# Kernel tuning notes

Measured on AMD Instinct MI355X. Metric: run time of the kernel, lower is better.

## Reference

```python
import jax, jax.numpy as jnp
import numpy as np

L, S, M, N, E, H = 1024, 1024, 256, 8, 512, 8


def embed_rotary(x, cos, sin):
    # x: [B, T, E]; interleaved rotate-half as in RotaryPositionEncoding.embed_rotary
    x2 = jnp.stack([-x[..., 1::2], x[..., 0::2]], axis=-1).reshape(x.shape)
    return x * cos + x2 * sin


def setup_inputs() -> dict:
    key = jax.random.key(0)
    ks = jax.random.split(key, 12)
    return {
        "query": jax.random.normal(ks[0], (L, N, E), jnp.float32),
        "key": jax.random.normal(ks[1], (S, N, E), jnp.float32),
        "value": jax.random.normal(ks[2], (S, N, E), jnp.float32),
        "in_proj_weight": jax.random.normal(ks[3], (3 * E, E), jnp.float32) / np.sqrt(E).astype(np.float32),
        "in_proj_bias": jnp.zeros((3 * E,), jnp.float32),
        "out_proj_weight": jax.random.normal(ks[4], (E, E), jnp.float32) / np.sqrt(E).astype(np.float32),
        "out_proj_bias": jnp.zeros((E,), jnp.float32),
        "rot_q": jax.random.normal(ks[5], (N, L, E, 2), jnp.float32),
        "rot_k": jax.random.normal(ks[6], (N, S, E, 2), jnp.float32),
        "k_mem": jax.random.normal(ks[7], (M, N, E), jnp.float32),
        "v_mem": jax.random.normal(ks[8], (M, N, E), jnp.float32),
        "gate_attn": jax.random.normal(ks[9], (H,), jnp.float32),
        "mem_mask": jax.random.randint(ks[10], (N, M), 0, 2).astype(bool),
        "num_heads": H,
    }


def reference(query, key, value, in_proj_weight, in_proj_bias, out_proj_weight,
              out_proj_bias, rot_q, rot_k, k_mem, v_mem, gate_attn, mem_mask, num_heads):
    L_, N_, E_ = query.shape
    S_ = key.shape[0]
    H_ = num_heads
    hd = E_ // H_
    scale = float(hd) ** -0.5
    # separate q/k/v projections (qkv not identical path)
    q = query @ in_proj_weight[:E_].T + in_proj_bias[:E_]
    k = key @ in_proj_weight[E_:2 * E_].T + in_proj_bias[E_:2 * E_]
    v = value @ in_proj_weight[2 * E_:].T + in_proj_bias[2 * E_:]
    q = q * scale
    # inline rotary PE (applied in batch-first layout, then back)
    q = embed_rotary(q.transpose(1, 0, 2), rot_q[..., 0], rot_q[..., 1]).transpose(1, 0, 2)
    k = embed_rotary(k.transpose(1, 0, 2), rot_k[..., 0], rot_k[..., 1]).transpose(1, 0, 2)
    qh = q.reshape(L_, N_, H_, hd).transpose(1, 2, 0, 3)  # [N,H,L,hd]
    kh = k.reshape(S_, N_, H_, hd).transpose(1, 2, 0, 3)  # [N,H,S,hd]
    vh = v.reshape(S_, N_, H_, hd).transpose(1, 2, 0, 3)
    scores = jnp.einsum('nhld,nhsd->nhls', qh, kh)
    # slot-competition: softmax over queries (slots), then renormalize over keys
    w = jax.nn.softmax(scores, axis=2) + 1e-8
    w = w / w.sum(axis=-1, keepdims=True)
    attn = jnp.einsum('nhls,nhsd->nhld', w, vh)
    # memorizing-transformer style memory K/V branch with sigmoid head gating
    Mm = k_mem.shape[0]
    km = k_mem.reshape(Mm, N_, H_, hd).transpose(1, 2, 0, 3)  # [N,H,M,hd]
    vm = v_mem.reshape(Mm, N_, H_, hd).transpose(1, 2, 0, 3)
    sm = jnp.einsum('nhld,nhmd->nhlm', qh, km)
    sm = jnp.where(mem_mask[:, None, None, :], -1e9, sm)  # additive -inf mask
    wm = jax.nn.softmax(sm, axis=-1)
    om = jnp.einsum('nhlm,nhmd->nhld', wm, vm)
    gate = jax.nn.sigmoid(gate_attn)[None, :, None, None]  # [1,H,1,1]
    attn = gate * om + (1.0 - gate) * attn
    out = attn.transpose(2, 0, 1, 3).reshape(L_, N_, E_)  # back to [L,N,E]
    return out @ out_proj_weight.T + out_proj_bias
```

## Files before the change

kernel.cpp:

```cpp
#include <hip/hip_runtime.h>
#include <hip/hip_bf16.h>

typedef __hip_bfloat16 bf16;
typedef __bf16 bf16x8 __attribute__((ext_vector_type(8)));
typedef float f32x4 __attribute__((ext_vector_type(4)));

#define LQ 1024
#define SK 1024
#define MMEM 256
#define NB 8
#define EE 512
#define NH 8
#define HD 64
#define NBH 64

__device__ inline __bf16 tobf(float f) {
  __hip_bfloat16 h = __float2bfloat16(f);
  return *reinterpret_cast<__bf16*>(&h);
}
__device__ inline float bf2f(__bf16 x) {
  unsigned short u; __builtin_memcpy(&u, &x, 2);
  unsigned int v = (unsigned int)u << 16;
  float f; __builtin_memcpy(&f, &v, 4);
  return f;
}
__device__ inline f32x4 MFMA(bf16x8 a, bf16x8 b, f32x4 c) {
  return __builtin_amdgcn_mfma_f32_16x16x32_bf16(a, b, c, 0, 0, 0);
}

__device__ inline void gload_lds16(const bf16* g, void* l) {
  __builtin_amdgcn_global_load_lds(
      (const __attribute__((address_space(1))) void*)g,
      (__attribute__((address_space(3))) void*)l, 16, 0, 0);
}

__device__ inline bf16x8 load8(const float* p) {
  float4 a = *(const float4*)p;
  float4 b = *(const float4*)(p + 4);
  bf16x8 r;
  r[0] = tobf(a.x); r[1] = tobf(a.y); r[2] = tobf(a.z); r[3] = tobf(a.w);
  r[4] = tobf(b.x); r[5] = tobf(b.y); r[6] = tobf(b.z); r[7] = tobf(b.w);
  return r;
}

#define CVT_T0 524288
#define CVT_T3 98304
#define CVT_T4 32768
__global__ __launch_bounds__(256) void convert5(
    const float* __restrict__ q, const float* __restrict__ k,
    const float* __restrict__ v, const float* __restrict__ w,
    const float* __restrict__ o, bf16* __restrict__ qc, bf16* __restrict__ kc,
    bf16* __restrict__ vc, bf16* __restrict__ wc, bf16* __restrict__ oc)
{
  long long t = (long long)blockIdx.x * 256 + threadIdx.x;
  const float* src; bf16* dst; long long idx;
  if (t < CVT_T0)               { src = q; dst = qc; idx = t; }
  else if (t < 2 * CVT_T0)      { src = k; dst = kc; idx = t - CVT_T0; }
  else if (t < 3 * CVT_T0)      { src = v; dst = vc; idx = t - 2 * CVT_T0; }
  else if (t < 3 * CVT_T0 + CVT_T3) { src = w; dst = wc; idx = t - 3 * CVT_T0; }
  else                          { src = o; dst = oc; idx = t - 3 * CVT_T0 - CVT_T3; }
  *(bf16x8*)(dst + idx * 8) = load8(src + idx * 8);
}

__global__ __launch_bounds__(256) void gemm_proj3(
    const bf16* __restrict__ qc, const bf16* __restrict__ kc,
    const bf16* __restrict__ vc, const bf16* __restrict__ ipwb,
    const float* __restrict__ ipb, bf16* __restrict__ pq,
    bf16* __restrict__ pk, bf16* __restrict__ v_raw)
{
  __shared__ __align__(16) char smem[33792];
  __bf16* As = (__bf16*)smem;
  __bf16* Bs = (__bf16*)(smem + 16384);
  const int z = blockIdx.z;
  const bf16* A = (z == 0) ? qc : (z == 1) ? kc : vc;
  const bf16* W = ipwb + (long long)z * EE * EE;
  const float* bias = ipb + z * EE;
  const float alpha = (z == 0) ? 0.125f : 1.f;
  const int bid2 = blockIdx.y * gridDim.x + blockIdx.x;
  const int xcd = bid2 & 7, sub = bid2 >> 3;
  const int by = (xcd << 3) + (sub >> 2);
  const int bx = sub & 3;
  const int tm0 = by << 7, tn0 = bx << 7;
  const int t = threadIdx.x;
  const int wave = t >> 6, lane = t & 63;
  const int wrow0 = (wave & 1) << 6, wcol0 = (wave >> 1) << 6;
  const int m16 = lane & 15, quad = lane >> 4;

  const f32x4 zero = {0.f, 0.f, 0.f, 0.f};
  f32x4 acc[4][4];
#pragma unroll
  for (int mi = 0; mi < 4; ++mi)
#pragma unroll
    for (int ni = 0; ni < 4; ++ni) acc[mi][ni] = zero;

  const bf16* Ab = A + (long long)tm0 * EE;
  const bf16* Bb = W + (long long)tn0 * EE;
  const int ob_u = wave << 10;

  for (int k0 = 0; k0 < EE; k0 += 64) {
#pragma unroll
    for (int c = 0; c < 4; ++c) {
      int ob = (c << 12) + ob_u;
      int obl = ob + (lane << 4);
      int row = obl >> 7;
      int ce = (obl & 127) >> 1;
      gload_lds16(Ab + (long long)row * EE + k0 + ce, smem + ob);
      gload_lds16(Bb + (long long)row * EE + k0 + ce, smem + 16384 + ob);
    }
    __syncthreads();
#pragma unroll
    for (int kh = 0; kh < 2; ++kh) {
      bf16x8 av[4], bv[4];
#pragma unroll
      for (int i = 0; i < 4; ++i) {
        av[i] = *(bf16x8*)(As + ((wrow0 + (i << 4) + m16) << 6) + (kh << 5) + (quad << 3));
        bv[i] = *(bf16x8*)(Bs + ((wcol0 + (i << 4) + m16) << 6) + (kh << 5) + (quad << 3));
      }
#pragma unroll
      for (int mi = 0; mi < 4; ++mi)
#pragma unroll
        for (int ni = 0; ni < 4; ++ni)
          acc[mi][ni] = MFMA(av[mi], bv[ni], acc[mi][ni]);
    }
    __syncthreads();
  }

  __bf16 (*Cs)[132] = (__bf16(*)[132])smem;
#pragma unroll
  for (int mi = 0; mi < 4; ++mi)
#pragma unroll
    for (int ni = 0; ni < 4; ++ni) {
      int col = wcol0 + (ni << 4) + m16;
      float bv = bias[tn0 + col];
#pragma unroll
      for (int r = 0; r < 4; ++r)
        Cs[wrow0 + (mi << 4) + (quad << 2) + r][col] =
            tobf((acc[mi][ni][r] + bv) * alpha);
    }
  __syncthreads();
  bf16* O = (z == 0) ? pq : (z == 1) ? pk : v_raw;
  const int crow = t >> 1, ch0 = (t & 1) << 6;
  long long gb = (long long)(tm0 + crow) * EE + tn0 + ch0;
#pragma unroll
  for (int j = 0; j < 64; j += 8)
    *(uint4*)(O + gb + j) = *(uint4*)&Cs[crow][ch0 + j];
}

__global__ __launch_bounds__(256) void rotary_kernel(
    const bf16* __restrict__ pq, const bf16* __restrict__ pk,
    const float* __restrict__ rot_q, const float* __restrict__ rot_k,
    bf16* __restrict__ Qh, bf16* __restrict__ Kh)
{
  const bf16* src = blockIdx.y ? pk : pq;
  const float* rot = blockIdx.y ? rot_k : rot_q;
  bf16* dst = blockIdx.y ? Kh : Qh;
  const int t = threadIdx.x;
  const int row = (blockIdx.x << 2) + (t >> 6);
  const int e0 = (t & 63) << 3;
  const int l = row >> 3, n = row & 7;
  bf16x8 x = *(const bf16x8*)(src + (long long)row * EE + e0);
  const float* rp = rot + ((((long long)n * LQ + l) * EE + e0) << 1);
  __bf16 vals[8];
#pragma unroll
  for (int j = 0; j < 8; j += 2) {
    float4 cs4 = *(const float4*)(rp + (j << 1));
    float x0 = bf2f(x[j]);
    float x1 = bf2f(x[j + 1]);
    vals[j]     = tobf(x0 * cs4.x - x1 * cs4.y);
    vals[j + 1] = tobf(x1 * cs4.z + x0 * cs4.w);
  }
  const int h = e0 >> 6, d0 = e0 & 63;
  *(uint4*)(dst + (((long long)(n * NH + h) * LQ + l) * HD + d0)) = *(uint4*)vals;
}

__global__ __launch_bounds__(256) void colsum_kernel(
    const bf16* __restrict__ Qh, const bf16* __restrict__ Kh,
    float* __restrict__ csum)
{
  __shared__ __align__(16) char QdB[16384];
  __shared__ float cpart[128][2];
  const int bid = blockIdx.y * gridDim.x + blockIdx.x;
  const int xcd = bid & 7, sub = bid >> 3;
  const int b = (xcd << 3) + (sub >> 3);
  const int st0 = (sub & 7) << 7;
  const int t = threadIdx.x;
  const int wave = t >> 6, lane = t & 63;
  const int wm = (wave & 1) << 5, wn = (wave >> 1) << 5;
  const int m16 = lane & 15, quad = lane >> 4;
  const int swz = (m16 & 7) << 4;

  bf16x8 bk[2][2][2];
#pragma unroll
  for (int g = 0; g < 2; ++g)
#pragma unroll
    for (int ni = 0; ni < 2; ++ni)
#pragma unroll
      for (int kh = 0; kh < 2; ++kh)
        bk[g][ni][kh] = *(const bf16x8*)(
            Kh + ((long long)b * SK + st0 + (g << 6) + wn + (ni << 4) + m16) * HD
               + (kh << 5) + (quad << 3));

  int ldsoff[2]; const bf16* qsrc[2];
#pragma unroll
  for (int c = 0; c < 2; ++c) {
    int tb = (wave << 11) + (c << 10) + (lane << 4);
    int row = tb >> 7, cb = tb & 127;
    int srcb = cb ^ ((row & 7) << 4);
    ldsoff[c] = (wave << 11) + (c << 10);
    qsrc[c] = Qh + ((long long)b * LQ + row) * HD + (srcb >> 1);
  }
#pragma unroll
  for (int c = 0; c < 2; ++c) gload_lds16(qsrc[c], QdB + ldsoff[c]);
  __syncthreads();

  const f32x4 zero = {0.f, 0.f, 0.f, 0.f};
  float colp[2][2] = {{0.f, 0.f}, {0.f, 0.f}};
  int cur = 0;
  for (int lt = 0; lt < 16; ++lt) {
    if (lt < 15) {
#pragma unroll
      for (int c = 0; c < 2; ++c)
        gload_lds16(qsrc[c] + (long long)(lt + 1) * 64 * HD,
                    QdB + ((cur ^ 1) << 13) + ldsoff[c]);
    }
    bf16x8 a0k[2], a1k[2];
#pragma unroll
    for (int kh = 0; kh < 2; ++kh) {
      int byt = ((kh << 6) + (quad << 4)) ^ swz;
      a0k[kh] = *(bf16x8*)(QdB + (cur << 13) + (wm + m16) * 128 + byt);
      a1k[kh] = *(bf16x8*)(QdB + (cur << 13) + (wm + 16 + m16) * 128 + byt);
    }
    f32x4 s[2][2][2];
#pragma unroll
    for (int g = 0; g < 2; ++g)
#pragma unroll
      for (int mi = 0; mi < 2; ++mi)
#pragma unroll
        for (int ni = 0; ni < 2; ++ni) s[g][mi][ni] = zero;
    __builtin_amdgcn_s_setprio(1);
#pragma unroll
    for (int g = 0; g < 2; ++g)
#pragma unroll
      for (int kh = 0; kh < 2; ++kh) {
        s[g][0][0] = MFMA(a0k[kh], bk[g][0][kh], s[g][0][0]);
        s[g][0][1] = MFMA(a0k[kh], bk[g][1][kh], s[g][0][1]);
        s[g][1][0] = MFMA(a1k[kh], bk[g][0][kh], s[g][1][0]);
        s[g][1][1] = MFMA(a1k[kh], bk[g][1][kh], s[g][1][1]);
      }
    __builtin_amdgcn_s_setprio(0);
#pragma unroll
    for (int g = 0; g < 2; ++g)
#pragma unroll
      for (int mi = 0; mi < 2; ++mi)
#pragma unroll
        for (int ni = 0; ni < 2; ++ni)
#pragma unroll
          for (int r = 0; r < 4; ++r)
            colp[g][ni] += __expf(s[g][mi][ni][r]);
    __syncthreads();
    cur ^= 1;
  }
#pragma unroll
  for (int g = 0; g < 2; ++g)
#pragma unroll
    for (int ni = 0; ni < 2; ++ni) {
      float v = colp[g][ni];
      v += __shfl_down(v, 32, 64);
      v += __shfl_down(v, 16, 64);
      if (quad == 0) cpart[(g << 6) + wn + (ni << 4) + m16][wm >> 5] = v;
    }
  __syncthreads();
  if (t < 128) csum[b * SK + st0 + t] = cpart[t][0] + cpart[t][1];
}

__global__ __launch_bounds__(256) void attn_fused(
    const bf16* __restrict__ Qh, const bf16* __restrict__ Kh,
    const bf16* __restrict__ Vt, const bf16* __restrict__ km,
    const bf16* __restrict__ vmt, const float* __restrict__ csum,
    const float* __restrict__ Vsum, const int* __restrict__ mask,
    const float* __restrict__ gate, bf16* __restrict__ comb)
{
  __shared__ __align__(16) char KdB[16384];
  __shared__ __align__(16) char VdB[16384];
  __shared__ __align__(16) char PsB[8192];
  __shared__ __align__(16) float rcs[SK];
  __shared__ __align__(16) float mskf[MMEM];
  __shared__ float rpa[64][2];
  __shared__ float rpm[64][2];
  const int bid = blockIdx.y * gridDim.x + blockIdx.x;
  const int xcd = bid & 7, sub = bid >> 3;
  const int b = (xcd << 3) + (sub >> 4);
  const int tm0 = (sub & 15) << 6;
  const int n = b >> 3, h = b & 7;
  const int t = threadIdx.x;
  const int lrow = t >> 2, lcol = (t & 3) << 4;
  const int wave = t >> 6, lane = t & 63;
  const int wm = (wave & 1) << 5, wn = (wave >> 1) << 5;
  const int m16 = lane & 15, quad = lane >> 4;
  const int swz = (m16 & 7) << 4;

#pragma unroll
  for (int i = 0; i < 4; ++i)
    rcs[t + i * 256] = 1.f / csum[b * SK + t + i * 256];
  mskf[t] = mask[n * MMEM + t] ? 0.f : 1.f;

  bf16x8 aq[2][2];
#pragma unroll
  for (int li = 0; li < 2; ++li)
#pragma unroll
    for (int kh = 0; kh < 2; ++kh)
      aq[li][kh] = *(const bf16x8*)(
          Qh + ((long long)b * LQ + tm0 + wm + (li << 4) + m16) * HD
             + (kh << 5) + (quad << 3));

  int ldsoff[2]; int srow[2], scol[2];
#pragma unroll
  for (int c = 0; c < 2; ++c) {
    int tb = (wave << 11) + (c << 10) + (lane << 4);
    int row = tb >> 7, cb = tb & 127;
    int srcb = cb ^ ((row & 7) << 4);
    ldsoff[c] = (wave << 11) + (c << 10);
    srow[c] = row; scol[c] = srcb >> 1;
  }
  const bf16* kmain = Kh + (long long)b * SK * HD;
  const bf16* vmain = Vt + (long long)b * HD * SK;
  const bf16* kmem = km + (long long)b * MMEM * HD;
  const bf16* vmem = vmt + (long long)b * HD * MMEM;

#pragma unroll
  for (int c = 0; c < 2; ++c) {
    gload_lds16(kmem + (long long)srow[c] * HD + scol[c], KdB + ldsoff[c]);
    gload_lds16(vmem + (long long)srow[c] * MMEM + scol[c], VdB + ldsoff[c]);
  }
  __syncthreads();

  const f32x4 zero = {0.f, 0.f, 0.f, 0.f};
  f32x4 m00 = zero, m01 = zero, m10 = zero, m11 = zero;
  f32x4 o00 = zero, o01 = zero, o10 = zero, o11 = zero;
  float rsm[2] = {0.f, 0.f};
  float rsa[2] = {0.f, 0.f};
  int cur = 0;

  for (int mt = 0; mt < 4; ++mt) {
    if (mt < 3) {
#pragma unroll
      for (int c = 0; c < 2; ++c) {
        gload_lds16(kmem + ((long long)((mt + 1) << 6) + srow[c]) * HD + scol[c],
                    KdB + ((cur ^ 1) << 13) + ldsoff[c]);
        gload_lds16(vmem + (long long)srow[c] * MMEM + ((mt + 1) << 6) + scol[c],
                    VdB + ((cur ^ 1) << 13) + ldsoff[c]);
      }
    } else {
#pragma unroll
      for (int c = 0; c < 2; ++c) {
        gload_lds16(kmain + (long long)srow[c] * HD + scol[c],
                    KdB + ((cur ^ 1) << 13) + ldsoff[c]);
        gload_lds16(vmain + (long long)srow[c] * SK + scol[c],
                    VdB + ((cur ^ 1) << 13) + ldsoff[c]);
      }
    }
    f32x4 s00 = zero, s01 = zero, s10 = zero, s11 = zero;
    __builtin_amdgcn_s_setprio(1);
#pragma unroll
    for (int kh = 0; kh < 2; ++kh) {
      int byt = ((kh << 6) + (quad << 4)) ^ swz;
      bf16x8 ak0 = *(bf16x8*)(KdB + (cur << 13) + (wn + m16) * 128 + byt);
      bf16x8 ak1 = *(bf16x8*)(KdB + (cur << 13) + (wn + 16 + m16) * 128 + byt);
      s00 = MFMA(ak0, aq[0][kh], s00);
      s01 = MFMA(ak0, aq[1][kh], s01);
      s10 = MFMA(ak1, aq[0][kh], s10);
      s11 = MFMA(ak1, aq[1][kh], s11);
    }
    __builtin_amdgcn_s_setprio(0);
    {
      char* pA = PsB + (wm + m16) * 128;
      char* pB = PsB + (wm + 16 + m16) * 128;
#pragma unroll
      for (int si = 0; si < 2; ++si) {
        int sloc = wn + (si << 4) + (quad << 2);
        f32x4 mf4 = *(const f32x4*)&mskf[(mt << 6) + sloc];
        f32x4 sA = si ? s10 : s00;
        f32x4 sB = si ? s11 : s01;
        __bf16 vA[4], vB[4];
#pragma unroll
        for (int r = 0; r < 4; ++r) {
          float pa = __expf(sA[r]) * mf4[r];
          rsm[0] += pa; vA[r] = tobf(pa);
          float pb = __expf(sB[r]) * mf4[r];
          rsm[1] += pb; vB[r] = tobf(pb);
        }
        int sbyte = (sloc << 1) ^ swz;
        *(uint2*)(pA + sbyte) = *(uint2*)vA;
        *(uint2*)(pB + sbyte) = *(uint2*)vB;
      }
    }
    __syncthreads();
    __builtin_amdgcn_s_setprio(1);
#pragma unroll
    for (int kh = 0; kh < 2; ++kh) {
      int sb = (kh << 6) + (quad << 4);
      int byt = sb ^ swz;
      bf16x8 ap0 = *(bf16x8*)(PsB + (wm + m16) * 128 + byt);
      bf16x8 ap1 = *(bf16x8*)(PsB + (wm + 16 + m16) * 128 + byt);
      bf16x8 bv0 = *(bf16x8*)(VdB + (cur << 13) + (wn + m16) * 128 + byt);
      bf16x8 bv1 = *(bf16x8*)(VdB + (cur << 13) + (wn + 16 + m16) * 128 + byt);
      m00 = MFMA(ap0, bv0, m00);
      m01 = MFMA(ap0, bv1, m01);
      m10 = MFMA(ap1, bv0, m10);
      m11 = MFMA(ap1, bv1, m11);
    }
    __builtin_amdgcn_s_setprio(0);
    __syncthreads();
    cur ^= 1;
  }

  for (int st = 0; st < 16; ++st) {
    if (st < 15) {
#pragma unroll
      for (int c = 0; c < 2; ++c) {
        gload_lds16(kmain + ((long long)((st + 1) << 6) + srow[c]) * HD + scol[c],
                    KdB + ((cur ^ 1) << 13) + ldsoff[c]);
        gload_lds16(vmain + (long long)srow[c] * SK + ((st + 1) << 6) + scol[c],
                    VdB + ((cur ^ 1) << 13) + ldsoff[c]);
      }
    }
    f32x4 s00 = zero, s01 = zero, s10 = zero, s11 = zero;
    __builtin_amdgcn_s_setprio(1);
#pragma unroll
    for (int kh = 0; kh < 2; ++kh) {
      int byt = ((kh << 6) + (quad << 4)) ^ swz;
      bf16x8 ak0 = *(bf16x8*)(KdB + (cur << 13) + (wn + m16) * 128 + byt);
      bf16x8 ak1 = *(bf16x8*)(KdB + (cur << 13) + (wn + 16 + m16) * 128 + byt);
      s00 = MFMA(ak0, aq[0][kh], s00);
      s01 = MFMA(ak0, aq[1][kh], s01);
      s10 = MFMA(ak1, aq[0][kh], s10);
      s11 = MFMA(ak1, aq[1][kh], s11);
    }
    __builtin_amdgcn_s_setprio(0);
    {
      char* pA = PsB + (wm + m16) * 128;
      char* pB = PsB + (wm + 16 + m16) * 128;
#pragma unroll
      for (int si = 0; si < 2; ++si) {
        int sloc = wn + (si << 4) + (quad << 2);
        f32x4 rc4 = *(const f32x4*)&rcs[(st << 6) + sloc];
        f32x4 sA = si ? s10 : s00;
        f32x4 sB = si ? s11 : s01;
        __bf16 vA[4], vB[4];
#pragma unroll
        for (int r = 0; r < 4; ++r) {
          float pa = __expf(sA[r]) * rc4[r];
          rsa[0] += pa; vA[r] = tobf(pa);
          float pb = __expf(sB[r]) * rc4[r];
          rsa[1] += pb; vB[r] = tobf(pb);
        }
        int sbyte = (sloc << 1) ^ swz;
        *(uint2*)(pA + sbyte) = *(uint2*)vA;
        *(uint2*)(pB + sbyte) = *(uint2*)vB;
      }
    }
    __syncthreads();
    __builtin_amdgcn_s_setprio(1);
#pragma unroll
    for (int kh = 0; kh < 2; ++kh) {
      int sb = (kh << 6) + (quad << 4);
      int byt = sb ^ swz;
      bf16x8 ap0 = *(bf16x8*)(PsB + (wm + m16) * 128 + byt);
      bf16x8 ap1 = *(bf16x8*)(PsB + (wm + 16 + m16) * 128 + byt);
      bf16x8 bv0 = *(bf16x8*)(VdB + (cur << 13) + (wn + m16) * 128 + byt);
      bf16x8 bv1 = *(bf16x8*)(VdB + (cur << 13) + (wn + 16 + m16) * 128 + byt);
      o00 = MFMA(ap0, bv0, o00);
      o01 = MFMA(ap0, bv1, o01);
      o10 = MFMA(ap1, bv0, o10);
      o11 = MFMA(ap1, bv1, o11);
    }
    __builtin_amdgcn_s_setprio(0);
    __syncthreads();
    cur ^= 1;
  }

#pragma unroll
  for (int li = 0; li < 2; ++li) {
    float va = rsa[li];
    va += __shfl_xor(va, 16, 64);
    va += __shfl_xor(va, 32, 64);
    float vm = rsm[li];
    vm += __shfl_xor(vm, 16, 64);
    vm += __shfl_xor(vm, 32, 64);
    if (quad == 0) {
      rpa[wm + (li << 4) + m16][wn >> 5] = va;
      rpm[wm + (li << 4) + m16][wn >> 5] = vm;
    }
  }
  __syncthreads();

  const float* vs = Vsum + b * HD;
  const float g = 1.f / (1.f + __expf(-gate[h]));
  f32x4 oacc[2][2] = {{o00, o01}, {o10, o11}};
  f32x4 macc[2][2] = {{m00, m01}, {m10, m11}};
  for (int mi = 0; mi < 2; ++mi)
    for (int ni = 0; ni < 2; ++ni) {
      int col = wn + (ni << 4) + m16;
      float vsc = 1e-8f * vs[col];
      for (int r = 0; r < 4; ++r) {
        int row = wm + (mi << 4) + (quad << 2) + r;
        float ra = rpa[row][0] + rpa[row][1];
        float rm = rpm[row][0] + rpm[row][1];
        float oa = (oacc[mi][ni][r] + vsc) / (ra + (float)SK * 1e-8f);
        float om = macc[mi][ni][r] / rm;
        *(__bf16*)(PsB + row * 128 + (((col << 1) ^ ((row & 7) << 4)))) =
            tobf(g * om + (1.f - g) * oa);
      }
    }
  __syncthreads();
  uint4 u0 = *(uint4*)(PsB + lrow * 128 + (((lcol << 1)) ^ ((lrow & 7) << 4)));
  uint4 u1 = *(uint4*)(PsB + lrow * 128 + ((((lcol + 8) << 1)) ^ ((lrow & 7) << 4)));
  long long gb = ((long long)b * LQ + tm0 + lrow) * HD + lcol;
  *(uint4*)(comb + gb) = u0;
  *(uint4*)(comb + gb + 8) = u1;
}

__global__ __launch_bounds__(256) void gemm_out(
    const bf16* __restrict__ comb, const bf16* __restrict__ opwb,
    const float* __restrict__ opb, float* __restrict__ out)
{
  __shared__ __align__(16) char smem[32768];
  __bf16* As = (__bf16*)smem;
  __bf16* Bs = (__bf16*)(smem + 16384);
  const int bid2 = blockIdx.y * gridDim.x + blockIdx.x;
  const int xcd = bid2 & 7, sub = bid2 >> 3;
  const int by = (xcd << 3) + (sub >> 2);
  const int bx = sub & 3;
  const int tm0 = by << 7, tn0 = bx << 7;
  const int t = threadIdx.x;
  const int wave = t >> 6, lane = t & 63;
  const int wrow0 = (wave & 1) << 6, wcol0 = (wave >> 1) << 6;
  const int m16 = lane & 15, quad = lane >> 4;

  const f32x4 zero = {0.f, 0.f, 0.f, 0.f};
  f32x4 acc[4][4];
#pragma unroll
  for (int mi = 0; mi < 4; ++mi)
#pragma unroll
    for (int ni = 0; ni < 4; ++ni) acc[mi][ni] = zero;

  const bf16* Bb = opwb + (long long)tn0 * EE;
  const int ob_u = wave << 10;

  for (int k0 = 0; k0 < EE; k0 += 64) {
    const int h = k0 >> 6;
#pragma unroll
    for (int c = 0; c < 4; ++c) {
      int ob = (c << 12) + ob_u;
      int obl = ob + (lane << 4);
      int row = obl >> 7;
      int ce = (obl & 127) >> 1;
      int arow = tm0 + row;
      int l = arow >> 3, nn = arow & 7;
      gload_lds16(comb + (((long long)(nn * NH + h) * LQ + l) * HD + ce),
                  smem + ob);
      gload_lds16(Bb + (long long)row * EE + k0 + ce, smem + 16384 + ob);
    }
    __syncthreads();
#pragma unroll
    for (int kh = 0; kh < 2; ++kh) {
      bf16x8 av[4], bv[4];
#pragma unroll
      for (int i = 0; i < 4; ++i) {
        av[i] = *(bf16x8*)(As + ((wrow0 + (i << 4) + m16) << 6) + (kh << 5) + (quad << 3));
        bv[i] = *(bf16x8*)(Bs + ((wcol0 + (i << 4) + m16) << 6) + (kh << 5) + (quad << 3));
      }
#pragma unroll
      for (int mi = 0; mi < 4; ++mi)
#pragma unroll
        for (int ni = 0; ni < 4; ++ni)
          acc[mi][ni] = MFMA(av[mi], bv[ni], acc[mi][ni]);
    }
    __syncthreads();
  }

#pragma unroll
  for (int mi = 0; mi < 4; ++mi)
#pragma unroll
    for (int ni = 0; ni < 4; ++ni) {
      int col = tn0 + wcol0 + (ni << 4) + m16;
      float bv = opb[col];
      int row0 = tm0 + wrow0 + (mi << 4) + (quad << 2);
#pragma unroll
      for (int r = 0; r < 4; ++r)
        out[(long long)(row0 + r) * EE + col] = acc[mi][ni][r] + bv;
    }
}

__global__ __launch_bounds__(256) void v_transpose(
    const bf16* __restrict__ raw, bf16* __restrict__ Vt,
    float* __restrict__ Vsum)
{
  __shared__ __align__(16) __bf16 Ts[64][72];
  const int bh = blockIdx.y;
  const int n = bh >> 3, h = bh & 7;
  const int s0 = blockIdx.x << 6;
  const int t = threadIdx.x;
  const int i = t >> 2, c0 = (t & 3) << 4;
  const bf16* rp = raw + ((long long)(s0 + i) * NB + n) * EE + h * HD + c0;
  *(bf16x8*)&Ts[i][c0] = *(const bf16x8*)rp;
  *(bf16x8*)&Ts[i][c0 + 8] = *(const bf16x8*)(rp + 8);
  __syncthreads();
  const int d = t >> 2, j0 = (t & 3) << 4;
  __bf16 vals[16];
  float part = 0.f;
#pragma unroll
  for (int j = 0; j < 16; ++j) { vals[j] = Ts[j0 + j][d]; part += bf2f(vals[j]); }
  bf16* wp = Vt + ((long long)bh * HD + d) * SK + s0 + j0;
  *(uint4*)wp = *(uint4*)&vals[0];
  *(uint4*)(wp + 8) = *(uint4*)&vals[8];
  part += __shfl_xor(part, 1, 64);
  part += __shfl_xor(part, 2, 64);
  if ((t & 3) == 0) atomicAdd(&Vsum[bh * HD + d], part);
}

__global__ __launch_bounds__(256) void mem_prep(
    const float* __restrict__ k_mem, const float* __restrict__ v_mem,
    bf16* __restrict__ km, bf16* __restrict__ vmt)
{
  __shared__ __align__(16) __bf16 Ts[64][72];
  const int bh = blockIdx.y;
  const int n = bh >> 3, h = bh & 7;
  const int m0 = blockIdx.x << 6;
  const int t = threadIdx.x;
  const int i = t >> 2, c0 = (t & 3) << 4;
  const float* kp = k_mem + ((long long)(m0 + i) * NB + n) * EE + h * HD + c0;
  const float* vp = v_mem + ((long long)(m0 + i) * NB + n) * EE + h * HD + c0;
  bf16x8 kv0 = load8(kp), kv1 = load8(kp + 8);
  bf16x8 vv0 = load8(vp), vv1 = load8(vp + 8);
  bf16* kw = km + ((long long)bh * MMEM + m0 + i) * HD + c0;
  *(bf16x8*)kw = kv0;
  *(bf16x8*)(kw + 8) = kv1;
  *(bf16x8*)&Ts[i][c0] = vv0;
  *(bf16x8*)&Ts[i][c0 + 8] = vv1;
  __syncthreads();
  const int d = t >> 2, j0 = (t & 3) << 4;
  __bf16 vals[16];
#pragma unroll
  for (int j = 0; j < 16; ++j) vals[j] = Ts[j0 + j][d];
  bf16* wp = vmt + ((long long)bh * HD + d) * MMEM + m0 + j0;
  *(uint4*)wp = *(uint4*)&vals[0];
  *(uint4*)(wp + 8) = *(uint4*)&vals[8];
}

extern "C" void kernel_launch(void* const* d_in, const int* in_sizes, int n_in,
                              void* d_out, int out_size, void* d_ws, size_t ws_size,
                              hipStream_t stream) {
  const float* query = (const float*)d_in[0];
  const float* key   = (const float*)d_in[1];
  const float* value = (const float*)d_in[2];
  const float* ipw   = (const float*)d_in[3];
  const float* ipb   = (const float*)d_in[4];
  const float* opw   = (const float*)d_in[5];
  const float* opb   = (const float*)d_in[6];
  const float* rot_q = (const float*)d_in[7];
  const float* rot_k = (const float*)d_in[8];
  const float* k_mem = (const float*)d_in[9];
  const float* v_mem = (const float*)d_in[10];
  const float* gate  = (const float*)d_in[11];
  const int*  mask   = (const int*)d_in[12];
  float* out = (float*)d_out;

  char* w = (char*)d_ws;
  size_t off = 0;
  auto carve = [&](size_t bytes) -> char* {
    char* p = w + off;
    off += (bytes + 255) & ~(size_t)255;
    return p;
  };
  bf16* qc    = (bf16*)carve((size_t)LQ * NB * EE * 2);
  bf16* kc    = (bf16*)carve((size_t)SK * NB * EE * 2);
  bf16* vc    = (bf16*)carve((size_t)SK * NB * EE * 2);
  bf16* ipwb  = (bf16*)carve((size_t)3 * EE * EE * 2);
  bf16* opwb  = (bf16*)carve((size_t)EE * EE * 2);
  bf16* v_raw = (bf16*)carve((size_t)SK * NB * EE * 2);
  bf16* Qh    = (bf16*)carve((size_t)NBH * LQ * HD * 2);
  bf16* Kh    = (bf16*)carve((size_t)NBH * SK * HD * 2);
  bf16* Vt    = (bf16*)carve((size_t)NBH * HD * SK * 2);
  bf16* km    = (bf16*)carve((size_t)NBH * MMEM * HD * 2);
  bf16* vmt   = (bf16*)carve((size_t)NBH * HD * MMEM * 2);
  float* csum = (float*)carve((size_t)NBH * SK * 4);
  float* Vsum = (float*)carve((size_t)NBH * HD * 4);
  bf16* comb  = (bf16*)carve((size_t)NBH * LQ * HD * 2);
  bf16* pkbuf = (bf16*)carve((size_t)NBH * LQ * HD * 2);
  if (off > ws_size) {
    hipMemsetAsync(d_out, 0, (size_t)out_size * 4, stream);
    return;
  }
  bf16* pq = comb;
  bf16* pk = pkbuf;

  convert5<<<(3 * CVT_T0 + CVT_T3 + CVT_T4) / 256, 256, 0, stream>>>(
      query, key, value, ipw, opw, qc, kc, vc, ipwb, opwb);
  hipMemsetAsync(Vsum, 0, (size_t)NBH * HD * 4, stream);

  gemm_proj3<<<dim3(EE / 128, (LQ * NB) / 128, 3), 256, 0, stream>>>(
      qc, kc, vc, ipwb, ipb, pq, pk, v_raw);

  rotary_kernel<<<dim3((LQ * NB) / 4, 2), 256, 0, stream>>>(
      pq, pk, rot_q, rot_k, Qh, Kh);

  v_transpose<<<dim3(SK / 64, NBH), 256, 0, stream>>>(v_raw, Vt, Vsum);
  mem_prep<<<dim3(MMEM / 64, NBH), 256, 0, stream>>>(k_mem, v_mem, km, vmt);

  colsum_kernel<<<dim3(SK / 128, NBH), 256, 0, stream>>>(Qh, Kh, csum);

  attn_fused<<<dim3(LQ / 64, NBH), 256, 0, stream>>>(
      Qh, Kh, Vt, km, vmt, csum, Vsum, mask, gate, comb);

  gemm_out<<<dim3(4, 64), 256, 0, stream>>>(comb, opwb, opb, out);
}
```

Baseline: 305.2 us.

## Restructure attention so each wave owns 16 query rows with register-staged prefetch

Reworks the fused attention kernel so each wave processes its own 16 query rows against all 64 keys per tile. The P tile now lives in a per-wave LDS region, which removes the block-wide barrier between the score and PV stages and the cross-wave row-sum reduction through shared memory. The direct global-to-LDS loads are replaced by register-staged prefetch of the next K/V tile, written to a double buffer after compute. The memory and main loops are merged into one non-unrolled loop. This cuts synchronisation but doubles the K/V LDS footprint to 64 KB, which may lower occupancy and raise register pressure.

```diff
diff --git a/kernel.cpp b/kernel.cpp
--- a/kernel.cpp
+++ b/kernel.cpp
@@ -280,13 +280,11 @@
     const float* __restrict__ Vsum, const int* __restrict__ mask,
     const float* __restrict__ gate, bf16* __restrict__ comb)
 {
-  __shared__ __align__(16) char KdB[16384];
-  __shared__ __align__(16) char VdB[16384];
+  __shared__ __align__(16) char KdB[32768];
+  __shared__ __align__(16) char VdB[32768];
   __shared__ __align__(16) char PsB[8192];
   __shared__ __align__(16) float rcs[SK];
   __shared__ __align__(16) float mskf[MMEM];
-  __shared__ float rpa[64][2];
-  __shared__ float rpm[64][2];
   const int bid = blockIdx.y * gridDim.x + blockIdx.x;
   const int xcd = bid & 7, sub = bid >> 3;
   const int b = (xcd << 3) + (sub >> 4);
@@ -295,229 +293,147 @@
   const int t = threadIdx.x;
   const int lrow = t >> 2, lcol = (t & 3) << 4;
   const int wave = t >> 6, lane = t & 63;
-  const int wm = (wave & 1) << 5, wn = (wave >> 1) << 5;
   const int m16 = lane & 15, quad = lane >> 4;
+  char* Pw = PsB + (wave << 11);
   const int swz = (m16 & 7) << 4;
+  const int stb0 = lrow * 128 + (((lcol << 1)) ^ ((lrow & 7) << 4));
+  const int stb1 = lrow * 128 + ((((lcol << 1) + 16)) ^ ((lrow & 7) << 4));
 
 #pragma unroll
   for (int i = 0; i < 4; ++i)
     rcs[t + i * 256] = 1.f / csum[b * SK + t + i * 256];
   mskf[t] = mask[n * MMEM + t] ? 0.f : 1.f;
 
-  bf16x8 aq[2][2];
-#pragma unroll
-  for (int li = 0; li < 2; ++li)
+  bf16x8 aq[2];
+#pragma unroll
+  for (int kh = 0; kh < 2; ++kh)
+    aq[kh] = *(const bf16x8*)(
+        Qh + ((long long)b * LQ + tm0 + (wave << 4) + m16) * HD
+           + (kh << 5) + (quad << 3));
+
+  const bf16* kmem = km + ((long long)b * MMEM + lrow) * HD + lcol;
+  const bf16* vmem = vmt + ((long long)b * HD + lrow) * MMEM + lcol;
+  const bf16* kmain = Kh + ((long long)b * SK + lrow) * HD + lcol;
+  const bf16* vmain = Vt + ((long long)b * HD + lrow) * SK + lcol;
+
+  {
+    bf16x8 k0 = *(const bf16x8*)kmem;
+    bf16x8 k1 = *(const bf16x8*)(kmem + 8);
+    bf16x8 v0 = *(const bf16x8*)vmem;
+    bf16x8 v1 = *(const bf16x8*)(vmem + 8);
+    *(bf16x8*)(KdB + stb0) = k0;  *(bf16x8*)(KdB + stb1) = k1;
+    *(bf16x8*)(VdB + stb0) = v0;  *(bf16x8*)(VdB + stb1) = v1;
+  }
+  __syncthreads();
+
+  const f32x4 zero = {0.f, 0.f, 0.f, 0.f};
+  f32x4 macc[4] = {zero, zero, zero, zero};
+  f32x4 oacc[4] = {zero, zero, zero, zero};
+  float rsm = 0.f, rsa = 0.f;
+  int cur = 0;
+
+#pragma unroll 1
+  for (int it = 0; it < 20; ++it) {
+    const bool mem = (it < 4);
+    bf16x8 kr0, kr1, vr0, vr1;
+    if (it < 19) {
+      const bf16 *kp, *vp;
+      if (it < 3)      { kp = kmem + (long long)((it + 1) << 6) * HD;
+                         vp = vmem + ((it + 1) << 6); }
+      else if (it == 3){ kp = kmain; vp = vmain; }
+      else             { kp = kmain + (long long)((it - 3) << 6) * HD;
+                         vp = vmain + ((it - 3) << 6); }
+      kr0 = *(const bf16x8*)kp;  kr1 = *(const bf16x8*)(kp + 8);
+      vr0 = *(const bf16x8*)vp;  vr1 = *(const bf16x8*)(vp + 8);
+    }
+    f32x4 sfr[4] = {zero, zero, zero, zero};
+    __builtin_amdgcn_s_setprio(1);
+#pragma unroll
+    for (int g = 0; g < 4; ++g)
+#pragma unroll
+      for (int kh = 0; kh < 2; ++kh) {
+        bf16x8 ak = *(bf16x8*)(KdB + (cur << 14) + ((g << 4) + m16) * 128 +
+                               (((kh << 6) + (quad << 4)) ^ swz));
+        sfr[g] = MFMA(ak, aq[kh], sfr[g]);
+      }
+    __builtin_amdgcn_s_setprio(0);
+    const float* scl = mem ? &mskf[(it << 6)] : &rcs[((it - 4) << 6)];
+#pragma unroll
+    for (int g = 0; g < 4; ++g) {
+      int s0 = (g << 4) + (quad << 2);
+      f32x4 sc = *(const f32x4*)(scl + s0);
+      __bf16 v4[4];
+#pragma unroll
+      for (int r = 0; r < 4; ++r) {
+        float p = __expf(sfr[g][r]) * sc[r];
+        if (mem) rsm += p; else rsa += p;
+        v4[r] = tobf(p);
+      }
+      *(uint2*)(Pw + m16 * 128 + (((s0 << 1)) ^ swz)) = *(uint2*)v4;
+    }
+    asm volatile("s_waitcnt lgkmcnt(0)" ::: "memory");
+    __builtin_amdgcn_sched_barrier(0);
+    bf16x8 ap[2];
 #pragma unroll
     for (int kh = 0; kh < 2; ++kh)
-      aq[li][kh] = *(const bf16x8*)(
-          Qh + ((long long)b * LQ + tm0 + wm + (li << 4) + m16) * HD
-             + (kh << 5) + (quad << 3));
-
-  int ldsoff[2]; int srow[2], scol[2];
-#pragma unroll
-  for (int c = 0; c < 2; ++c) {
-    int tb = (wave << 11) + (c << 10) + (lane << 4);
-    int row = tb >> 7, cb = tb & 127;
-    int srcb = cb ^ ((row & 7) << 4);
-    ldsoff[c] = (wave << 11) + (c << 10);
-    srow[c] = row; scol[c] = srcb >> 1;
-  }
-  const bf16* kmain = Kh + (long long)b * SK * HD;
-  const bf16* vmain = Vt + (long long)b * HD * SK;
-  const bf16* kmem = km + (long long)b * MMEM * HD;
-  const bf16* vmem = vmt + (long long)b * HD * MMEM;
-
-#pragma unroll
-  for (int c = 0; c < 2; ++c) {
-    gload_lds16(kmem + (long long)srow[c] * HD + scol[c], KdB + ldsoff[c]);
-    gload_lds16(vmem + (long long)srow[c] * MMEM + scol[c], VdB + ldsoff[c]);
-  }
-  __syncthreads();
-
-  const f32x4 zero = {0.f, 0.f, 0.f, 0.f};
-  f32x4 m00 = zero, m01 = zero, m10 = zero, m11 = zero;
-  f32x4 o00 = zero, o01 = zero, o10 = zero, o11 = zero;
-  float rsm[2] = {0.f, 0.f};
-  float rsa[2] = {0.f, 0.f};
-  int cur = 0;
-
-  for (int mt = 0; mt < 4; ++mt) {
-    if (mt < 3) {
-#pragma unroll
-      for (int c = 0; c < 2; ++c) {
-        gload_lds16(kmem + ((long long)((mt + 1) << 6) + srow[c]) * HD + scol[c],
-                    KdB + ((cur ^ 1) << 13) + ldsoff[c]);
-        gload_lds16(vmem + (long long)srow[c] * MMEM + ((mt + 1) << 6) + scol[c],
-                    VdB + ((cur ^ 1) << 13) + ldsoff[c]);
+      ap[kh] = *(bf16x8*)(Pw + m16 * 128 + (((kh << 6) + (quad << 4)) ^ swz));
+    __builtin_amdgcn_s_setprio(1);
+#pragma unroll
+    for (int dfr = 0; dfr < 4; ++dfr)
+#pragma unroll
+      for (int kh = 0; kh < 2; ++kh) {
+        bf16x8 bv = *(bf16x8*)(VdB + (cur << 14) + ((dfr << 4) + m16) * 128 +
+                               (((kh << 6) + (quad << 4)) ^ swz));
+        if (mem) macc[dfr] = MFMA(ap[kh], bv, macc[dfr]);
+        else     oacc[dfr] = MFMA(ap[kh], bv, oacc[dfr]);
       }
-    } else {
-#pragma unroll
-      for (int c = 0; c < 2; ++c) {
-        gload_lds16(kmain + (long long)srow[c] * HD + scol[c],
-                    KdB + ((cur ^ 1) << 13) + ldsoff[c]);
-        gload_lds16(vmain + (long long)srow[c] * SK + scol[c],
-                    VdB + ((cur ^ 1) << 13) + ldsoff[c]);
-      }
-    }
-    f32x4 s00 = zero, s01 = zero, s10 = zero, s11 = zero;
-    __builtin_amdgcn_s_setprio(1);
-#pragma unroll
-    for (int kh = 0; kh < 2; ++kh) {
-      int byt = ((kh << 6) + (quad << 4)) ^ swz;
-      bf16x8 ak0 = *(bf16x8*)(KdB + (cur << 13) + (wn + m16) * 128 + byt);
-      bf16x8 ak1 = *(bf16x8*)(KdB + (cur << 13) + (wn + 16 + m16) * 128 + byt);
-      s00 = MFMA(ak0, aq[0][kh], s00);
-      s01 = MFMA(ak0, aq[1][kh], s01);
-      s10 = MFMA(ak1, aq[0][kh], s10);
-      s11 = MFMA(ak1, aq[1][kh], s11);
-    }
     __builtin_amdgcn_s_setprio(0);
-    {
-      char* pA = PsB + (wm + m16) * 128;
-      char* pB = PsB + (wm + 16 + m16) * 128;
-#pragma unroll
-      for (int si = 0; si < 2; ++si) {
-        int sloc = wn + (si << 4) + (quad << 2);
-        f32x4 mf4 = *(const f32x4*)&mskf[(mt << 6) + sloc];
-        f32x4 sA = si ? s10 : s00;
-        f32x4 sB = si ? s11 : s01;
-        __bf16 vA[4], vB[4];
-#pragma unroll
-        for (int r = 0; r < 4; ++r) {
-          float pa = __expf(sA[r]) * mf4[r];
-          rsm[0] += pa; vA[r] = tobf(pa);
-          float pb = __expf(sB[r]) * mf4[r];
-          rsm[1] += pb; vB[r] = tobf(pb);
-        }
-        int sbyte = (sloc << 1) ^ swz;
-        *(uint2*)(pA + sbyte) = *(uint2*)vA;
-        *(uint2*)(pB + sbyte) = *(uint2*)vB;
-      }
-    }
-    __syncthreads();
-    __builtin_amdgcn_s_setprio(1);
-#pragma unroll
-    for (int kh = 0; kh < 2; ++kh) {
-      int sb = (kh << 6) + (quad << 4);
-      int byt = sb ^ swz;
-      bf16x8 ap0 = *(bf16x8*)(PsB + (wm + m16) * 128 + byt);
-      bf16x8 ap1 = *(bf16x8*)(PsB + (wm + 16 + m16) * 128 + byt);
-      bf16x8 bv0 = *(bf16x8*)(VdB + (cur << 13) + (wn + m16) * 128 + byt);
-      bf16x8 bv1 = *(bf16x8*)(VdB + (cur << 13) + (wn + 16 + m16) * 128 + byt);
-      m00 = MFMA(ap0, bv0, m00);
-      m01 = MFMA(ap0, bv1, m01);
-      m10 = MFMA(ap1, bv0, m10);
-      m11 = MFMA(ap1, bv1, m11);
-    }
-    __builtin_amdgcn_s_setprio(0);
+    if (it < 19) {
+      *(bf16x8*)(KdB + ((cur ^ 1) << 14) + stb0) = kr0;
+      *(bf16x8*)(KdB + ((cur ^ 1) << 14) + stb1) = kr1;
+      *(bf16x8*)(VdB + ((cur ^ 1) << 14) + stb0) = vr0;
+      *(bf16x8*)(VdB + ((cur ^ 1) << 14) + stb1) = vr1;
+    }
     __syncthreads();
     cur ^= 1;
   }
 
-  for (int st = 0; st < 16; ++st) {
-    if (st < 15) {
-#pragma unroll
-      for (int c = 0; c < 2; ++c) {
-        gload_lds16(kmain + ((long long)((st + 1) << 6) + srow[c]) * HD + scol[c],
-                    KdB + ((cur ^ 1) << 13) + ldsoff[c]);
-        gload_lds16(vmain + (long long)srow[c] * SK + ((st + 1) << 6) + scol[c],
-                    VdB + ((cur ^ 1) << 13) + ldsoff[c]);
-      }
-    }
-    f32x4 s00 = zero, s01 = zero, s10 = zero, s11 = zero;
-    __builtin_amdgcn_s_setprio(1);
-#pragma unroll
-    for (int kh = 0; kh < 2; ++kh) {
-      int byt = ((kh << 6) + (quad << 4)) ^ swz;
-      bf16x8 ak0 = *(bf16x8*)(KdB + (cur << 13) + (wn + m16) * 128 + byt);
-      bf16x8 ak1 = *(bf16x8*)(KdB + (cur << 13) + (wn + 16 + m16) * 128 + byt);
-      s00 = MFMA(ak0, aq[0][kh], s00);
-      s01 = MFMA(ak0, aq[1][kh], s01);
-      s10 = MFMA(ak1, aq[0][kh], s10);
-      s11 = MFMA(ak1, aq[1][kh], s11);
-    }
-    __builtin_amdgcn_s_setprio(0);
-    {
-      char* pA = PsB + (wm + m16) * 128;
-      char* pB = PsB + (wm + 16 + m16) * 128;
-#pragma unroll
-      for (int si = 0; si < 2; ++si) {
-        int sloc = wn + (si << 4) + (quad << 2);
-        f32x4 rc4 = *(const f32x4*)&rcs[(st << 6) + sloc];
-        f32x4 sA = si ? s10 : s00;
-        f32x4 sB = si ? s11 : s01;
-        __bf16 vA[4], vB[4];
-#pragma unroll
-        for (int r = 0; r < 4; ++r) {
-          float pa = __expf(sA[r]) * rc4[r];
-          rsa[0] += pa; vA[r] = tobf(pa);
-          float pb = __expf(sB[r]) * rc4[r];
-          rsa[1] += pb; vB[r] = tobf(pb);
-        }
-        int sbyte = (sloc << 1) ^ swz;
-        *(uint2*)(pA + sbyte) = *(uint2*)vA;
-        *(uint2*)(pB + sbyte) = *(uint2*)vB;
-      }
-    }
-    __syncthreads();
-    __builtin_amdgcn_s_setprio(1);
-#pragma unroll
-    for (int kh = 0; kh < 2; ++kh) {
-      int sb = (kh << 6) + (quad << 4);
-      int byt = sb ^ swz;
-      bf16x8 ap0 = *(bf16x8*)(PsB + (wm + m16) * 128 + byt);
-      bf16x8 ap1 = *(bf16x8*)(PsB + (wm + 16 + m16) * 128 + byt);
-      bf16x8 bv0 = *(bf16x8*)(VdB + (cur << 13) + (wn + m16) * 128 + byt);
-      bf16x8 bv1 = *(bf16x8*)(VdB + (cur << 13) + (wn + 16 + m16) * 128 + byt);
-      o00 = MFMA(ap0, bv0, o00);
-      o01 = MFMA(ap0, bv1, o01);
-      o10 = MFMA(ap1, bv0, o10);
-      o11 = MFMA(ap1, bv1, o11);
-    }
-    __builtin_amdgcn_s_setprio(0);
-    __syncthreads();
-    cur ^= 1;
-  }
-
-#pragma unroll
-  for (int li = 0; li < 2; ++li) {
-    float va = rsa[li];
-    va += __shfl_xor(va, 16, 64);
-    va += __shfl_xor(va, 32, 64);
-    float vm = rsm[li];
-    vm += __shfl_xor(vm, 16, 64);
-    vm += __shfl_xor(vm, 32, 64);
-    if (quad == 0) {
-      rpa[wm + (li << 4) + m16][wn >> 5] = va;
-      rpm[wm + (li << 4) + m16][wn >> 5] = vm;
-    }
-  }
-  __syncthreads();
-
-  const float* vs = Vsum + b * HD;
+  rsa += __shfl_xor(rsa, 16, 64);
+  rsa += __shfl_xor(rsa, 32, 64);
+  rsm += __shfl_xor(rsm, 16, 64);
+  rsm += __shfl_xor(rsm, 32, 64);
+
+  float raL[4], rmL[4];
+#pragma unroll
+  for (int r = 0; r < 4; ++r) {
+    raL[r] = __shfl(rsa, (quad << 2) + r, 64);
+    rmL[r] = __shfl(rsm, (quad << 2) + r, 64);
+  }
   const float g = 1.f / (1.f + __expf(-gate[h]));
-  f32x4 oacc[2][2] = {{o00, o01}, {o10, o11}};
-  f32x4 macc[2][2] = {{m00, m01}, {m10, m11}};
-  for (int mi = 0; mi < 2; ++mi)
-    for (int ni = 0; ni < 2; ++ni) {
-      int col = wn + (ni << 4) + m16;
-      float vsc = 1e-8f * vs[col];
-      for (int r = 0; r < 4; ++r) {
-        int row = wm + (mi << 4) + (quad << 2) + r;
-        float ra = rpa[row][0] + rpa[row][1];
-        float rm = rpm[row][0] + rpm[row][1];
-        float oa = (oacc[mi][ni][r] + vsc) / (ra + (float)SK * 1e-8f);
-        float om = macc[mi][ni][r] / rm;
-        *(__bf16*)(PsB + row * 128 + (((col << 1) ^ ((row & 7) << 4)))) =
-            tobf(g * om + (1.f - g) * oa);
-      }
-    }
-  __syncthreads();
-  uint4 u0 = *(uint4*)(PsB + lrow * 128 + (((lcol << 1)) ^ ((lrow & 7) << 4)));
-  uint4 u1 = *(uint4*)(PsB + lrow * 128 + ((((lcol + 8) << 1)) ^ ((lrow & 7) << 4)));
-  long long gb = ((long long)b * LQ + tm0 + lrow) * HD + lcol;
-  *(uint4*)(comb + gb) = u0;
-  *(uint4*)(comb + gb + 8) = u1;
+#pragma unroll
+  for (int dfr = 0; dfr < 4; ++dfr) {
+    int d = (dfr << 4) + m16;
+    float vsc = 1e-8f * Vsum[b * HD + d];
+#pragma unroll
+    for (int r = 0; r < 4; ++r) {
+      float oa = (oacc[dfr][r] + vsc) / (raL[r] + (float)SK * 1e-8f);
+      float om = macc[dfr][r] / rmL[r];
+      int row = (quad << 2) + r;
+      *(__bf16*)(Pw + row * 128 + (((d << 1)) ^ ((row & 7) << 4))) =
+          tobf(g * om + (1.f - g) * oa);
+    }
+  }
+  asm volatile("s_waitcnt lgkmcnt(0)" ::: "memory");
+  __builtin_amdgcn_sched_barrier(0);
+  {
+    int orow = lane >> 2, ocol = (lane & 3) << 4;
+    int osz = (orow & 7) << 4;
+    uint4 u0 = *(uint4*)(Pw + orow * 128 + (((ocol << 1)) ^ osz));
+    uint4 u1 = *(uint4*)(Pw + orow * 128 + ((((ocol << 1) + 16)) ^ osz));
+    long long gb = ((long long)b * LQ + tm0 + (wave << 4) + orow) * HD + ocol;
+    *(uint4*)(comb + gb) = u0;
+    *(uint4*)(comb + gb + 8) = u1;
+  }
 }
 
 __global__ __launch_bounds__(256) void gemm_out(
```

Result: slower. 328.5 us (+7.7%).
